# Performance work log

Measured on AMD Instinct MI355X. Metric: run time of the kernel, lower is better.

Reference implementation:

```python
import jax, jax.numpy as jnp
import numpy as np

UNITS = 128
N_CLASSES = 10
N_FEAT = 3
R_ON = 0.05      # time-gate open ratio
ALPHA = 0.001    # leak during closed phase
LN_EPS = 1e-3    # keras LayerNormalization default epsilon


def _time_gate(t, tau, s):
    # t: [B], tau/s: [U] -> k: [B, U]
    phi = jnp.mod(t[:, None] - s, tau) / tau
    k = jnp.where(phi < 0.5 * R_ON, 2.0 * phi / R_ON,
        jnp.where(phi < R_ON, 2.0 - 2.0 * phi / R_ON, ALPHA * phi))
    return k


def _plstm_step(x, t, h, c, Wx, Wh, b, tau, s):
    z = x @ Wx + h @ Wh + b                      # [B, 4U]
    i, f, g, o = jnp.split(z, 4, axis=-1)
    c_hat = jax.nn.sigmoid(f) * c + jax.nn.sigmoid(i) * jnp.tanh(g)
    h_hat = jax.nn.sigmoid(o) * jnp.tanh(c_hat)
    k = _time_gate(t, tau, s)
    return k * h_hat + (1.0 - k) * h, k * c_hat + (1.0 - k) * c


def _layer_norm(x, gamma, beta):
    mu = jnp.mean(x, axis=-1, keepdims=True)
    var = jnp.mean(jnp.square(x - mu), axis=-1, keepdims=True)
    return gamma * (x - mu) * jax.lax.rsqrt(var + LN_EPS) + beta


def setup_inputs() -> dict:
    key = jax.random.key(0)
    ks = jax.random.split(key, 16)
    B, T, F, U, C = 256, 1000, N_FEAT, UNITS, N_CLASSES
    inputs = jax.random.normal(ks[0], (B, T, F), dtype=jnp.float32)
    # strictly increasing-ish observation times per sequence
    times = jnp.cumsum(jax.random.uniform(ks[1], (B, T), dtype=jnp.float32), axis=1)
    sc_in = 1.0 / np.sqrt(F)
    sc_h = 1.0 / np.sqrt(U)
    Wx0 = jax.random.normal(ks[2], (F, 4 * U), dtype=jnp.float32) * sc_in
    Wh0 = jax.random.normal(ks[3], (U, 4 * U), dtype=jnp.float32) * sc_h
    b0 = jnp.zeros((4 * U,), dtype=jnp.float32)
    tau0 = jnp.exp(jax.random.uniform(ks[4], (U,), minval=0.0, maxval=3.0, dtype=jnp.float32))
    s0 = jax.random.uniform(ks[5], (U,), dtype=jnp.float32) * tau0
    Wx1 = jax.random.normal(ks[6], (U, 4 * U), dtype=jnp.float32) * sc_h
    Wh1 = jax.random.normal(ks[7], (U, 4 * U), dtype=jnp.float32) * sc_h
    b1 = jnp.zeros((4 * U,), dtype=jnp.float32)
    tau1 = jnp.exp(jax.random.uniform(ks[8], (U,), minval=0.0, maxval=3.0, dtype=jnp.float32))
    s1 = jax.random.uniform(ks[9], (U,), dtype=jnp.float32) * tau1
    gamma = jnp.ones((U,), dtype=jnp.float32)
    beta = jnp.zeros((U,), dtype=jnp.float32)
    Wfc = jax.random.normal(ks[10], (U, C), dtype=jnp.float32) * sc_h
    bfc = jnp.zeros((C,), dtype=jnp.float32)
    return {"inputs": inputs, "times": times, "Wx0": Wx0, "Wh0": Wh0, "b0": b0,
            "tau0": tau0, "s0": s0, "Wx1": Wx1, "Wh1": Wh1, "b1": b1,
            "tau1": tau1, "s1": s1, "gamma": gamma, "beta": beta,
            "Wfc": Wfc, "bfc": bfc}


def reference(inputs, times, Wx0, Wh0, b0, tau0, s0, Wx1, Wh1, b1, tau1, s1,
              gamma, beta, Wfc, bfc):
    B, T, F = inputs.shape
    U = Wh0.shape[0]
    x_t = jnp.transpose(inputs, (1, 0, 2))   # [T, B, F]
    t_t = jnp.transpose(times, (1, 0))       # [T, B]

    def step(carry, xt):
        h0, c0, h1, c1 = carry
        x, t = xt
        h0, c0 = _plstm_step(x, t, h0, c0, Wx0, Wh0, b0, tau0, s0)
        hn = _layer_norm(h0, gamma, beta)
        h1, c1 = _plstm_step(hn, t, h1, c1, Wx1, Wh1, b1, tau1, s1)
        probs = jax.nn.softmax(h1 @ Wfc + bfc, axis=-1)
        return (h0, c0, h1, c1), probs

    zeros = jnp.zeros((B, U), dtype=inputs.dtype)
    init = (zeros, zeros, zeros, zeros)
    _, out = jax.lax.scan(step, init, (x_t, t_t))  # out: [T, B, C]
    return jnp.transpose(out, (1, 0, 2))           # [B, T, C]
```

## Files before the change

kernel.cpp:

```cpp
#include <hip/hip_runtime.h>
#include <math.h>

constexpr int U      = 128;
constexpr int G4     = 512;
constexpr int NCls   = 10;
constexpr int TSTEPS = 1000;
constexpr int BATCH  = 256;
constexpr int CROWS  = 48;


__device__ __forceinline__ float sigm(float x) {
    return 1.0f / (1.0f + __expf(-x));
}

__device__ __forceinline__ float tgate(float t, float tau, float s) {
    float r = fmodf(t - s, tau);
    if (r < 0.0f) r += tau;
    const float phi = r / tau;
    return (phi < 0.025f) ? 40.0f * phi
         : (phi < 0.05f)  ? 2.0f - 40.0f * phi
         : 0.001f * phi;
}

#define ROW4(WP, I, HB) { \
    float4 w_; \
    w_ = (WP)[((I)+0)*128]; ac.x += (HB).x*w_.x; ac.y += (HB).x*w_.y; ac.z += (HB).x*w_.z; ac.w += (HB).x*w_.w; \
    w_ = (WP)[((I)+1)*128]; ac.x += (HB).y*w_.x; ac.y += (HB).y*w_.y; ac.z += (HB).y*w_.z; ac.w += (HB).y*w_.w; \
    w_ = (WP)[((I)+2)*128]; ac.x += (HB).z*w_.x; ac.y += (HB).z*w_.y; ac.z += (HB).z*w_.z; ac.w += (HB).z*w_.w; \
    w_ = (WP)[((I)+3)*128]; ac.x += (HB).w*w_.x; ac.y += (HB).w*w_.y; ac.z += (HB).w*w_.z; ac.w += (HB).w*w_.w; }

__global__ __launch_bounds__(1024, 1) void plstm_fused(
    const float* __restrict__ inputs,
    const float* __restrict__ times,
    const float* __restrict__ Wx0,
    const float* __restrict__ Wh0,
    const float* __restrict__ b0,
    const float* __restrict__ tau0,
    const float* __restrict__ s0,
    const float* __restrict__ Wx1,
    const float* __restrict__ Wh1,
    const float* __restrict__ b1,
    const float* __restrict__ tau1,
    const float* __restrict__ s1,
    const float* __restrict__ gamma_,
    const float* __restrict__ beta_,
    const float* __restrict__ Wfc,
    const float* __restrict__ bfc,
    float* __restrict__ out)
{
    const int tid = threadIdx.x;
    const int c4  = tid & 127;
    const int g   = tid >> 7;
    const int b   = blockIdx.x;

    __shared__ __align__(16) float wh0c[CROWS * G4];
    __shared__ __align__(16) float zu[8 * G4];
    __shared__ __align__(16) float h0s[U];
    __shared__ __align__(16) float ghu[2 * U];
    __shared__ __align__(16) float b0s[G4], b1s[G4], Ps[G4], Qs[G4];
    __shared__ __align__(16) float wx0s[3 * G4];
    __shared__ __align__(16) float wfcs[U * 11];
    __shared__ float bfcs[NCls];
    __shared__ float red[4];
    __shared__ float gms[U], bts[U];

    if (tid < U) { gms[tid] = gamma_[tid]; bts[tid] = beta_[tid];
                   h0s[tid] = 0.f; ghu[tid] = 0.f; ghu[U + tid] = 0.f; }
    {
        float4* dst = reinterpret_cast<float4*>(wh0c);
        const float4* src = reinterpret_cast<const float4*>(Wh0);
        #pragma unroll
        for (int i = 0; i < 6; ++i) dst[tid + i * 1024] = src[tid + i * 1024];
    }
    if (tid < G4) { b0s[tid] = b0[tid]; b1s[tid] = b1[tid]; }
    for (int i = tid; i < 3 * G4; i += 1024) wx0s[i] = Wx0[i];
    for (int i = tid; i < U * NCls; i += 1024) {
        const int u = i / NCls, c = i - u * NCls;
        wfcs[u * 11 + c] = Wfc[i];
    }
    if (tid < NCls) bfcs[tid] = bfc[tid];
    __syncthreads();

    if (tid < G4) {
        float P = 0.f, Q = 0.f;
        #pragma unroll 8
        for (int u = 0; u < U; ++u) {
            const float w = Wx1[u * G4 + tid];
            Q += gms[u] * w;
            P += bts[u] * w;
        }
        Ps[tid] = P; Qs[tid] = Q;
    }

    float tau0r = 0.f, s0r = 0.f, tau1r = 0.f, s1r = 0.f, gr = 0.f;
    if (tid < U) {
        tau0r = tau0[tid]; s0r = s0[tid];
        tau1r = tau1[tid]; s1r = s1[tid];
        gr = gms[tid];
    }
    float c0r = 0.f, c1r = 0.f, h0r = 0.f, h1r = 0.f;

    const float* __restrict__ xp = inputs + (size_t)b * TSTEPS * 3;
    const float* __restrict__ tp = times  + (size_t)b * TSTEPS;
    float*       __restrict__ op = out    + (size_t)b * TSTEPS * NCls;

    float xa0 = xp[0], xa1 = xp[1], xa2 = xp[2], tva = tp[0];

    __syncthreads();

    for (int t = 0; t < TSTEPS; ++t) {
        const float x0 = xa0, x1 = xa1, x2 = xa2, tv = tva;
        const int tn = (t + 1 < TSTEPS) ? t + 1 : t;
        xa0 = xp[tn*3+0]; xa1 = xp[tn*3+1]; xa2 = xp[tn*3+2]; tva = tp[tn];

        {
            float4 ac = make_float4(0.f, 0.f, 0.f, 0.f);
            const int r0 = g * 16;
            if (g < 3) {
                const float4* wp = reinterpret_cast<const float4*>(wh0c) + r0 * 128 + c4;
                #pragma unroll 2
                for (int i = 0; i < 16; i += 4) {
                    const float4 hb = *reinterpret_cast<const float4*>(&h0s[r0 + i]);
                    ROW4(wp, i, hb);
                }
            } else {
                const float4* wp = reinterpret_cast<const float4*>(Wh0) + r0 * 128 + c4;
                #pragma unroll 2
                for (int i = 0; i < 16; i += 4) {
                    const float4 hb = *reinterpret_cast<const float4*>(&h0s[r0 + i]);
                    ROW4(wp, i, hb);
                }
            }
            *reinterpret_cast<float4*>(&zu[g * G4 + 4 * c4]) = ac;
        }
        __syncthreads();

        if (tid < U) {
            const int u = tid;
            float z[4];
            #pragma unroll
            for (int q = 0; q < 4; ++q) {
                const int c = u + q * 128;
                float s = b0s[c] + x0 * wx0s[c] + x1 * wx0s[G4 + c] + x2 * wx0s[2 * G4 + c];
                #pragma unroll
                for (int gg = 0; gg < 8; ++gg) s += zu[gg * G4 + c];
                z[q] = s;
            }
            const float ig = sigm(z[0]);
            const float fg = sigm(z[1]);
            const float gg = tanhf(z[2]);
            const float og = sigm(z[3]);
            const float ch = fg * c0r + ig * gg;
            const float hh = og * tanhf(ch);
            const float k  = tgate(tv, tau0r, s0r);
            const float hn = k * hh + (1.0f - k) * h0r;
            c0r = k * ch + (1.0f - k) * c0r;
            h0r = hn;
            h0s[u] = hn;
            ghu[u] = gr * hn;
            float ssum = hn, qsum = hn * hn;
            #pragma unroll
            for (int off = 1; off < 64; off <<= 1) {
                ssum += __shfl_xor(ssum, off);
                qsum += __shfl_xor(qsum, off);
            }
            if ((tid & 63) == 0) {
                red[(tid >> 6) * 2]     = ssum;
                red[(tid >> 6) * 2 + 1] = qsum;
            }
        }
        __syncthreads();

        {
            const int half = tid >> 9;
            const int rg   = (tid >> 7) & 3;
            const int r0   = rg * 32;
            const float* __restrict__ Wm = half ? Wh1 : Wx1;
            const float* hvp = ghu + half * U + r0;
            const float4* wp = reinterpret_cast<const float4*>(Wm) + r0 * 128 + c4;
            float4 ac = make_float4(0.f, 0.f, 0.f, 0.f);
            #pragma unroll 2
            for (int i = 0; i < 32; i += 4) {
                const float4 hb = *reinterpret_cast<const float4*>(&hvp[i]);
                ROW4(wp, i, hb);
            }
            *reinterpret_cast<float4*>(&zu[(half * 4 + rg) * G4 + 4 * c4]) = ac;
        }
        __syncthreads();

        if (tid < U) {
            const float mu    = (red[0] + red[2]) * (1.0f / 128.0f);
            const float msq   = (red[1] + red[3]) * (1.0f / 128.0f);
            const float rstd  = rsqrtf(msq - mu * mu + 1e-3f);
            const float murstd = mu * rstd;
            const int u = tid;
            float z[4];
            #pragma unroll
            for (int q = 0; q < 4; ++q) {
                const int c = u + q * 128;
                const float sx = (zu[0*G4+c] + zu[1*G4+c]) + (zu[2*G4+c] + zu[3*G4+c]);
                const float sh = (zu[4*G4+c] + zu[5*G4+c]) + (zu[6*G4+c] + zu[7*G4+c]);
                z[q] = b1s[c] + Ps[c] + rstd * sx - murstd * Qs[c] + sh;
            }
            const float ig = sigm(z[0]);
            const float fg = sigm(z[1]);
            const float gg = tanhf(z[2]);
            const float og = sigm(z[3]);
            const float ch = fg * c1r + ig * gg;
            const float hh = og * tanhf(ch);
            const float k  = tgate(tv, tau1r, s1r);
            const float hn = k * hh + (1.0f - k) * h1r;
            c1r = k * ch + (1.0f - k) * c1r;
            h1r = hn;
            ghu[U + u] = hn;
        }
        __syncthreads();

        if (tid < 64) {
            const float a  = ghu[U + tid];
            const float bv = ghu[U + tid + 64];
            float p[NCls];
            #pragma unroll
            for (int c = 0; c < NCls; ++c)
                p[c] = a * wfcs[tid * 11 + c] + bv * wfcs[(tid + 64) * 11 + c];
            #pragma unroll
            for (int off = 1; off < 64; off <<= 1) {
                #pragma unroll
                for (int c = 0; c < NCls; ++c) p[c] += __shfl_xor(p[c], off);
            }
            float m = -1e30f;
            #pragma unroll
            for (int c = 0; c < NCls; ++c) { p[c] += bfcs[c]; m = fmaxf(m, p[c]); }
            float ssum = 0.0f;
            #pragma unroll
            for (int c = 0; c < NCls; ++c) { p[c] = __expf(p[c] - m); ssum += p[c]; }
            const float inv = 1.0f / ssum;
            float pv = p[0];
            #pragma unroll
            for (int c = 1; c < NCls; ++c) if (tid == c) pv = p[c];
            if (tid < NCls) op[t * NCls + tid] = pv * inv;
        }
    }
}

extern "C" void kernel_launch(void* const* d_in, const int* in_sizes, int n_in,
                              void* d_out, int out_size, void* d_ws, size_t ws_size,
                              hipStream_t stream) {
    const float* inputs = (const float*)d_in[0];
    const float* times  = (const float*)d_in[1];
    const float* Wx0    = (const float*)d_in[2];
    const float* Wh0    = (const float*)d_in[3];
    const float* b0     = (const float*)d_in[4];
    const float* tau0   = (const float*)d_in[5];
    const float* s0     = (const float*)d_in[6];
    const float* Wx1    = (const float*)d_in[7];
    const float* Wh1    = (const float*)d_in[8];
    const float* b1     = (const float*)d_in[9];
    const float* tau1   = (const float*)d_in[10];
    const float* s1     = (const float*)d_in[11];
    const float* gamma_ = (const float*)d_in[12];
    const float* beta_  = (const float*)d_in[13];
    const float* Wfc    = (const float*)d_in[14];
    const float* bfc    = (const float*)d_in[15];
    float* out = (float*)d_out;

    dim3 grid(BATCH);
    dim3 block(1024);
    hipLaunchKernelGGL(plstm_fused, grid, block, 0, stream,
                       inputs, times, Wx0, Wh0, b0, tau0, s0,
                       Wx1, Wh1, b1, tau1, s1, gamma_, beta_, Wfc, bfc, out);
}
```

Measured before the change: 7.087 ms.

## Prefetch global weight rows into registers before barriers and cache more Wh0 rows

Raises the number of Wh0 rows cached in shared memory from 48 to 56 and rebalances the row split: group 3 now takes rows 48-55 from shared memory plus rows 56-63 from preloaded registers. Groups that still read Wh0 from global memory issue the loads for their first 8 rows during the previous phase, before a barrier, so the latency overlaps other work. The same is done for the first 8 rows of Wx1/Wh1 in the layer-1 matvec, which are loaded before the barrier that precedes their use. This costs extra registers, about 64 floats per thread, and slightly more shared memory, which could cause spills at 1024 threads.

```diff
diff --git a/kernel.cpp b/kernel.cpp
--- a/kernel.cpp
+++ b/kernel.cpp
@@ -6,7 +6,7 @@
 constexpr int NCls   = 10;
 constexpr int TSTEPS = 1000;
 constexpr int BATCH  = 256;
-constexpr int CROWS  = 48;
+constexpr int CROWS  = 56;
 
 
 __device__ __forceinline__ float sigm(float x) {
@@ -28,6 +28,12 @@
     w_ = (WP)[((I)+1)*128]; ac.x += (HB).y*w_.x; ac.y += (HB).y*w_.y; ac.z += (HB).y*w_.z; ac.w += (HB).y*w_.w; \
     w_ = (WP)[((I)+2)*128]; ac.x += (HB).z*w_.x; ac.y += (HB).z*w_.y; ac.z += (HB).z*w_.z; ac.w += (HB).z*w_.w; \
     w_ = (WP)[((I)+3)*128]; ac.x += (HB).w*w_.x; ac.y += (HB).w*w_.y; ac.z += (HB).w*w_.z; ac.w += (HB).w*w_.w; }
+
+#define ROW4P(W0, W1, W2, W3, HB) { \
+    ac.x += (HB).x*(W0).x; ac.y += (HB).x*(W0).y; ac.z += (HB).x*(W0).z; ac.w += (HB).x*(W0).w; \
+    ac.x += (HB).y*(W1).x; ac.y += (HB).y*(W1).y; ac.z += (HB).y*(W1).z; ac.w += (HB).y*(W1).w; \
+    ac.x += (HB).z*(W2).x; ac.y += (HB).z*(W2).y; ac.z += (HB).z*(W2).z; ac.w += (HB).z*(W2).w; \
+    ac.x += (HB).w*(W3).x; ac.y += (HB).w*(W3).y; ac.z += (HB).w*(W3).z; ac.w += (HB).w*(W3).w; }
 
 __global__ __launch_bounds__(1024, 1) void plstm_fused(
     const float* __restrict__ inputs,
@@ -70,7 +76,7 @@
         float4* dst = reinterpret_cast<float4*>(wh0c);
         const float4* src = reinterpret_cast<const float4*>(Wh0);
         #pragma unroll
-        for (int i = 0; i < 6; ++i) dst[tid + i * 1024] = src[tid + i * 1024];
+        for (int i = 0; i < 7; ++i) dst[tid + i * 1024] = src[tid + i * 1024];
     }
     if (tid < G4) { b0s[tid] = b0[tid]; b1s[tid] = b1[tid]; }
     for (int i = tid; i < 3 * G4; i += 1024) wx0s[i] = Wx0[i];
@@ -100,11 +106,29 @@
     }
     float c0r = 0.f, c1r = 0.f, h0r = 0.f, h1r = 0.f;
 
+    const int paBase = (g == 3) ? 56 : g * 16;
+    const float4* __restrict__ wpA =
+        reinterpret_cast<const float4*>(Wh0) + paBase * 128 + c4;
+    const int half = tid >> 9;
+    const int rgC  = (tid >> 7) & 3;
+    const int r0C  = rgC * 32;
+    const float4* __restrict__ wpC =
+        reinterpret_cast<const float4*>(half ? Wh1 : Wx1) + r0C * 128 + c4;
+    const float* __restrict__ hvpC = ghu + half * U + r0C;
+
     const float* __restrict__ xp = inputs + (size_t)b * TSTEPS * 3;
     const float* __restrict__ tp = times  + (size_t)b * TSTEPS;
     float*       __restrict__ op = out    + (size_t)b * TSTEPS * NCls;
 
     float xa0 = xp[0], xa1 = xp[1], xa2 = xp[2], tva = tp[0];
+
+    float4 pa0, pa1, pa2, pa3, pa4, pa5, pa6, pa7;
+    if (g >= 3) {
+        pa0 = wpA[0 * 128]; pa1 = wpA[1 * 128];
+        pa2 = wpA[2 * 128]; pa3 = wpA[3 * 128];
+        pa4 = wpA[4 * 128]; pa5 = wpA[5 * 128];
+        pa6 = wpA[6 * 128]; pa7 = wpA[7 * 128];
+    }
 
     __syncthreads();
 
@@ -115,20 +139,33 @@
 
         {
             float4 ac = make_float4(0.f, 0.f, 0.f, 0.f);
-            const int r0 = g * 16;
             if (g < 3) {
-                const float4* wp = reinterpret_cast<const float4*>(wh0c) + r0 * 128 + c4;
-                #pragma unroll 2
+                const float4* wp = reinterpret_cast<const float4*>(wh0c) + g * 16 * 128 + c4;
+                #pragma unroll
                 for (int i = 0; i < 16; i += 4) {
-                    const float4 hb = *reinterpret_cast<const float4*>(&h0s[r0 + i]);
+                    const float4 hb = *reinterpret_cast<const float4*>(&h0s[g * 16 + i]);
                     ROW4(wp, i, hb);
                 }
             } else {
-                const float4* wp = reinterpret_cast<const float4*>(Wh0) + r0 * 128 + c4;
-                #pragma unroll 2
-                for (int i = 0; i < 16; i += 4) {
-                    const float4 hb = *reinterpret_cast<const float4*>(&h0s[r0 + i]);
-                    ROW4(wp, i, hb);
+                {
+                    const float4 hb0 = *reinterpret_cast<const float4*>(&h0s[paBase]);
+                    ROW4P(pa0, pa1, pa2, pa3, hb0);
+                    const float4 hb1 = *reinterpret_cast<const float4*>(&h0s[paBase + 4]);
+                    ROW4P(pa4, pa5, pa6, pa7, hb1);
+                }
+                if (g == 3) {
+                    const float4* wp = reinterpret_cast<const float4*>(wh0c) + 48 * 128 + c4;
+                    #pragma unroll
+                    for (int i = 0; i < 8; i += 4) {
+                        const float4 hb = *reinterpret_cast<const float4*>(&h0s[48 + i]);
+                        ROW4(wp, i, hb);
+                    }
+                } else {
+                    #pragma unroll
+                    for (int i = 8; i < 16; i += 4) {
+                        const float4 hb = *reinterpret_cast<const float4*>(&h0s[g * 16 + i]);
+                        ROW4(wpA, i, hb);
+                    }
                 }
             }
             *reinterpret_cast<float4*>(&zu[g * G4 + 4 * c4]) = ac;
@@ -169,22 +206,26 @@
                 red[(tid >> 6) * 2 + 1] = qsum;
             }
         }
+        const float4 pc0 = wpC[0 * 128], pc1 = wpC[1 * 128],
+                     pc2 = wpC[2 * 128], pc3 = wpC[3 * 128],
+                     pc4 = wpC[4 * 128], pc5 = wpC[5 * 128],
+                     pc6 = wpC[6 * 128], pc7 = wpC[7 * 128];
         __syncthreads();
 
         {
-            const int half = tid >> 9;
-            const int rg   = (tid >> 7) & 3;
-            const int r0   = rg * 32;
-            const float* __restrict__ Wm = half ? Wh1 : Wx1;
-            const float* hvp = ghu + half * U + r0;
-            const float4* wp = reinterpret_cast<const float4*>(Wm) + r0 * 128 + c4;
             float4 ac = make_float4(0.f, 0.f, 0.f, 0.f);
-            #pragma unroll 2
-            for (int i = 0; i < 32; i += 4) {
-                const float4 hb = *reinterpret_cast<const float4*>(&hvp[i]);
-                ROW4(wp, i, hb);
-            }
-            *reinterpret_cast<float4*>(&zu[(half * 4 + rg) * G4 + 4 * c4]) = ac;
+            {
+                const float4 hb0 = *reinterpret_cast<const float4*>(&hvpC[0]);
+                ROW4P(pc0, pc1, pc2, pc3, hb0);
+                const float4 hb1 = *reinterpret_cast<const float4*>(&hvpC[4]);
+                ROW4P(pc4, pc5, pc6, pc7, hb1);
+            }
+            #pragma unroll 3
+            for (int i = 8; i < 32; i += 4) {
+                const float4 hb = *reinterpret_cast<const float4*>(&hvpC[i]);
+                ROW4(wpC, i, hb);
+            }
+            *reinterpret_cast<float4*>(&zu[(half * 4 + rgC) * G4 + 4 * c4]) = ac;
         }
         __syncthreads();
 
@@ -213,6 +254,12 @@
             c1r = k * ch + (1.0f - k) * c1r;
             h1r = hn;
             ghu[U + u] = hn;
+        }
+        if (g >= 3) {
+            pa0 = wpA[0 * 128]; pa1 = wpA[1 * 128];
+            pa2 = wpA[2 * 128]; pa3 = wpA[3 * 128];
+            pa4 = wpA[4 * 128]; pa5 = wpA[5 * 128];
+            pa6 = wpA[6 * 128]; pa7 = wpA[7 * 128];
         }
         __syncthreads();
 
```

After: 15.54 ms. 2.19x slower.

## Software-pipeline layer-1 and softmax one step behind layer-0, cutting barriers per step

Applied to the files above, without the earlier changes.

Restructures the per-timestep schedule so layer-1's cell update and the softmax output for step t-1 run concurrently with layer-0's work for step t. All 16 wavefronts now do gate math: half handle layer 0 and half handle layer 1, each unit computed redundantly by paired wavefronts. Per-wave private h buffers (gh0w, h1w) and double zu buffers let the per-step barrier count drop from four to two. The shared-memory cache of Wh0 shrinks from 48 to 32 rows to make room for the extra buffers, so more Wh0 rows are read from global memory. The layer-norm statistics are now summed across duplicated wavefronts (hence the 1/256 divisor), and an epilogue finishes the last step.

```diff
diff --git a/kernel.cpp b/kernel.cpp
--- a/kernel.cpp
+++ b/kernel.cpp
@@ -6,7 +6,6 @@
 constexpr int NCls   = 10;
 constexpr int TSTEPS = 1000;
 constexpr int BATCH  = 256;
-constexpr int CROWS  = 48;
 
 
 __device__ __forceinline__ float sigm(float x) {
@@ -48,29 +47,37 @@
     const float* __restrict__ bfc,
     float* __restrict__ out)
 {
-    const int tid = threadIdx.x;
-    const int c4  = tid & 127;
-    const int g   = tid >> 7;
-    const int b   = blockIdx.x;
-
-    __shared__ __align__(16) float wh0c[CROWS * G4];
-    __shared__ __align__(16) float zu[8 * G4];
+    const int tid  = threadIdx.x;
+    const int lane = tid & 63;
+    const int wv   = tid >> 6;
+    const int c4   = tid & 127;
+    const int g    = tid >> 7;
+    const int half = tid >> 9;
+    const int rgC  = (tid >> 7) & 3;
+    const int b    = blockIdx.x;
+
+    __shared__ __align__(16) float wh0c[32 * G4];
+    __shared__ __align__(16) float zu0[8 * G4];
+    __shared__ __align__(16) float zu1[8 * G4];
     __shared__ __align__(16) float h0s[U];
-    __shared__ __align__(16) float ghu[2 * U];
+    __shared__ __align__(16) float h1s[U];
+    __shared__ __align__(16) float gh0w[8][32];
+    __shared__ __align__(16) float h1w[8][32];
     __shared__ __align__(16) float b0s[G4], b1s[G4], Ps[G4], Qs[G4];
     __shared__ __align__(16) float wx0s[3 * G4];
     __shared__ __align__(16) float wfcs[U * 11];
     __shared__ float bfcs[NCls];
-    __shared__ float red[4];
+    __shared__ float red[8];
     __shared__ float gms[U], bts[U];
 
     if (tid < U) { gms[tid] = gamma_[tid]; bts[tid] = beta_[tid];
-                   h0s[tid] = 0.f; ghu[tid] = 0.f; ghu[U + tid] = 0.f; }
+                   h0s[tid] = 0.f; h1s[tid] = 0.f; }
+    if (tid < 256) { ((float*)h1w)[tid] = 0.f; }
     {
         float4* dst = reinterpret_cast<float4*>(wh0c);
         const float4* src = reinterpret_cast<const float4*>(Wh0);
         #pragma unroll
-        for (int i = 0; i < 6; ++i) dst[tid + i * 1024] = src[tid + i * 1024];
+        for (int i = 0; i < 4; ++i) dst[tid + i * 1024] = src[tid + i * 1024];
     }
     if (tid < G4) { b0s[tid] = b0[tid]; b1s[tid] = b1[tid]; }
     for (int i = tid; i < 3 * G4; i += 1024) wx0s[i] = Wx0[i];
@@ -92,19 +99,28 @@
         Ps[tid] = P; Qs[tid] = Q;
     }
 
-    float tau0r = 0.f, s0r = 0.f, tau1r = 0.f, s1r = 0.f, gr = 0.f;
-    if (tid < U) {
-        tau0r = tau0[tid]; s0r = s0[tid];
-        tau1r = tau1[tid]; s1r = s1[tid];
-        gr = gms[tid];
-    }
-    float c0r = 0.f, c1r = 0.f, h0r = 0.f, h1r = 0.f;
+    const int rg0 = (half == 0) ? (wv >> 1) : 0;
+    const int rg1 = (half == 1) ? ((wv - 8) >> 1) : 0;
+    const int um  = ((half == 0) ? rg0 : rg1) * 32 + (lane & 31);
+    float tauM = 0.f, sM = 0.f, grM = 0.f;
+    if (half == 0) { tauM = tau0[um]; sM = s0[um]; grM = gamma_[um]; }
+    else           { tauM = tau1[um]; sM = s1[um]; }
+    float cM = 0.f, hM = 0.f;
+
+    const float4* __restrict__ wpA =
+        reinterpret_cast<const float4*>(Wh0) + g * 16 * 128 + c4;
+    const float4* __restrict__ wpAc =
+        reinterpret_cast<const float4*>(wh0c) + g * 16 * 128 + c4;
+    const float4* __restrict__ wpC =
+        reinterpret_cast<const float4*>(half ? Wh1 : Wx1) + rgC * 32 * 128 + c4;
+    const float* __restrict__ hvC = half ? &h1w[wv - 8][0] : &gh0w[wv][0];
 
     const float* __restrict__ xp = inputs + (size_t)b * TSTEPS * 3;
     const float* __restrict__ tp = times  + (size_t)b * TSTEPS;
     float*       __restrict__ op = out    + (size_t)b * TSTEPS * NCls;
 
     float xa0 = xp[0], xa1 = xp[1], xa2 = xp[2], tva = tp[0];
+    float tvp = 0.f;
 
     __syncthreads();
 
@@ -113,133 +129,150 @@
         const int tn = (t + 1 < TSTEPS) ? t + 1 : t;
         xa0 = xp[tn*3+0]; xa1 = xp[tn*3+1]; xa2 = xp[tn*3+2]; tva = tp[tn];
 
+        if (half == 1 && t > 0) {
+            const float mu   = (red[0]+red[2]+red[4]+red[6]) * (1.0f/256.0f);
+            const float msq  = (red[1]+red[3]+red[5]+red[7]) * (1.0f/256.0f);
+            const float rstd = rsqrtf(msq - mu*mu + 1e-3f);
+            const float murstd = mu * rstd;
+            float z[4];
+            #pragma unroll
+            for (int q = 0; q < 4; ++q) {
+                const int c = um + q * 128;
+                const float sx = (zu1[0*G4+c] + zu1[1*G4+c]) + (zu1[2*G4+c] + zu1[3*G4+c]);
+                const float sh = (zu1[4*G4+c] + zu1[5*G4+c]) + (zu1[6*G4+c] + zu1[7*G4+c]);
+                z[q] = b1s[c] + Ps[c] + rstd * sx - murstd * Qs[c] + sh;
+            }
+            const float ig = sigm(z[0]), fg = sigm(z[1]);
+            const float gg = tanhf(z[2]), og = sigm(z[3]);
+            const float ch = fg * cM + ig * gg;
+            const float hh = og * tanhf(ch);
+            const float k  = tgate(tvp, tauM, sM);
+            const float hn = k * hh + (1.0f - k) * hM;
+            cM = k * ch + (1.0f - k) * cM;
+            hM = hn;
+            if (lane < 32) { h1w[wv - 8][lane] = hn; h1s[um] = hn; }
+        }
         {
             float4 ac = make_float4(0.f, 0.f, 0.f, 0.f);
-            const int r0 = g * 16;
-            if (g < 3) {
-                const float4* wp = reinterpret_cast<const float4*>(wh0c) + r0 * 128 + c4;
-                #pragma unroll 2
-                for (int i = 0; i < 16; i += 4) {
-                    const float4 hb = *reinterpret_cast<const float4*>(&h0s[r0 + i]);
-                    ROW4(wp, i, hb);
-                }
-            } else {
-                const float4* wp = reinterpret_cast<const float4*>(Wh0) + r0 * 128 + c4;
-                #pragma unroll 2
-                for (int i = 0; i < 16; i += 4) {
-                    const float4 hb = *reinterpret_cast<const float4*>(&h0s[r0 + i]);
-                    ROW4(wp, i, hb);
-                }
-            }
-            *reinterpret_cast<float4*>(&zu[g * G4 + 4 * c4]) = ac;
+            const float4* wp = (g < 2) ? wpAc : wpA;
+            #pragma unroll
+            for (int i = 0; i < 16; i += 4) {
+                const float4 hb = *reinterpret_cast<const float4*>(&h0s[g * 16 + i]);
+                ROW4(wp, i, hb);
+            }
+            *reinterpret_cast<float4*>(&zu0[g * G4 + 4 * c4]) = ac;
         }
         __syncthreads();
 
-        if (tid < U) {
-            const int u = tid;
+        if (wv == 0 && t > 0) {
+            const float a  = h1s[lane];
+            const float bv = h1s[lane + 64];
+            float p[NCls];
+            #pragma unroll
+            for (int c = 0; c < NCls; ++c)
+                p[c] = a * wfcs[lane * 11 + c] + bv * wfcs[(lane + 64) * 11 + c];
+            #pragma unroll
+            for (int off = 1; off < 64; off <<= 1) {
+                #pragma unroll
+                for (int c = 0; c < NCls; ++c) p[c] += __shfl_xor(p[c], off);
+            }
+            float m = -1e30f;
+            #pragma unroll
+            for (int c = 0; c < NCls; ++c) { p[c] += bfcs[c]; m = fmaxf(m, p[c]); }
+            float ssum = 0.0f;
+            #pragma unroll
+            for (int c = 0; c < NCls; ++c) { p[c] = __expf(p[c] - m); ssum += p[c]; }
+            const float inv = 1.0f / ssum;
+            float pv = p[0];
+            #pragma unroll
+            for (int c = 1; c < NCls; ++c) if (lane == c) pv = p[c];
+            if (lane < NCls) op[(t - 1) * NCls + lane] = pv * inv;
+        }
+        if (half == 0) {
             float z[4];
             #pragma unroll
             for (int q = 0; q < 4; ++q) {
-                const int c = u + q * 128;
-                float s = b0s[c] + x0 * wx0s[c] + x1 * wx0s[G4 + c] + x2 * wx0s[2 * G4 + c];
-                #pragma unroll
-                for (int gg = 0; gg < 8; ++gg) s += zu[gg * G4 + c];
+                const int c = um + q * 128;
+                float s = b0s[c] + x0 * wx0s[c] + x1 * wx0s[G4 + c] + x2 * wx0s[2*G4 + c];
+                s += (zu0[0*G4+c] + zu0[1*G4+c]) + (zu0[2*G4+c] + zu0[3*G4+c]);
+                s += (zu0[4*G4+c] + zu0[5*G4+c]) + (zu0[6*G4+c] + zu0[7*G4+c]);
                 z[q] = s;
             }
-            const float ig = sigm(z[0]);
-            const float fg = sigm(z[1]);
-            const float gg = tanhf(z[2]);
-            const float og = sigm(z[3]);
-            const float ch = fg * c0r + ig * gg;
+            const float ig = sigm(z[0]), fg = sigm(z[1]);
+            const float gg = tanhf(z[2]), og = sigm(z[3]);
+            const float ch = fg * cM + ig * gg;
             const float hh = og * tanhf(ch);
-            const float k  = tgate(tv, tau0r, s0r);
-            const float hn = k * hh + (1.0f - k) * h0r;
-            c0r = k * ch + (1.0f - k) * c0r;
-            h0r = hn;
-            h0s[u] = hn;
-            ghu[u] = gr * hn;
+            const float k  = tgate(tv, tauM, sM);
+            const float hn = k * hh + (1.0f - k) * hM;
+            cM = k * ch + (1.0f - k) * cM;
+            hM = hn;
+            if (lane < 32) { h0s[um] = hn; gh0w[wv][lane] = grM * hn; }
             float ssum = hn, qsum = hn * hn;
             #pragma unroll
             for (int off = 1; off < 64; off <<= 1) {
                 ssum += __shfl_xor(ssum, off);
                 qsum += __shfl_xor(qsum, off);
             }
-            if ((tid & 63) == 0) {
-                red[(tid >> 6) * 2]     = ssum;
-                red[(tid >> 6) * 2 + 1] = qsum;
-            }
-        }
+            if (lane == 0) { red[2 * rg0] = ssum; red[2 * rg0 + 1] = qsum; }
+        }
+        {
+            float4 ac = make_float4(0.f, 0.f, 0.f, 0.f);
+            #pragma unroll 4
+            for (int i = 0; i < 32; i += 4) {
+                const float4 hb = *reinterpret_cast<const float4*>(&hvC[i]);
+                ROW4(wpC, i, hb);
+            }
+            *reinterpret_cast<float4*>(&zu1[(half * 4 + rgC) * G4 + 4 * c4]) = ac;
+        }
+        tvp = tv;
         __syncthreads();
-
-        {
-            const int half = tid >> 9;
-            const int rg   = (tid >> 7) & 3;
-            const int r0   = rg * 32;
-            const float* __restrict__ Wm = half ? Wh1 : Wx1;
-            const float* hvp = ghu + half * U + r0;
-            const float4* wp = reinterpret_cast<const float4*>(Wm) + r0 * 128 + c4;
-            float4 ac = make_float4(0.f, 0.f, 0.f, 0.f);
-            #pragma unroll 2
-            for (int i = 0; i < 32; i += 4) {
-                const float4 hb = *reinterpret_cast<const float4*>(&hvp[i]);
-                ROW4(wp, i, hb);
-            }
-            *reinterpret_cast<float4*>(&zu[(half * 4 + rg) * G4 + 4 * c4]) = ac;
-        }
-        __syncthreads();
-
-        if (tid < U) {
-            const float mu    = (red[0] + red[2]) * (1.0f / 128.0f);
-            const float msq   = (red[1] + red[3]) * (1.0f / 128.0f);
-            const float rstd  = rsqrtf(msq - mu * mu + 1e-3f);
-            const float murstd = mu * rstd;
-            const int u = tid;
-            float z[4];
-            #pragma unroll
-            for (int q = 0; q < 4; ++q) {
-                const int c = u + q * 128;
-                const float sx = (zu[0*G4+c] + zu[1*G4+c]) + (zu[2*G4+c] + zu[3*G4+c]);
-                const float sh = (zu[4*G4+c] + zu[5*G4+c]) + (zu[6*G4+c] + zu[7*G4+c]);
-                z[q] = b1s[c] + Ps[c] + rstd * sx - murstd * Qs[c] + sh;
-            }
-            const float ig = sigm(z[0]);
-            const float fg = sigm(z[1]);
-            const float gg = tanhf(z[2]);
-            const float og = sigm(z[3]);
-            const float ch = fg * c1r + ig * gg;
-            const float hh = og * tanhf(ch);
-            const float k  = tgate(tv, tau1r, s1r);
-            const float hn = k * hh + (1.0f - k) * h1r;
-            c1r = k * ch + (1.0f - k) * c1r;
-            h1r = hn;
-            ghu[U + u] = hn;
-        }
-        __syncthreads();
-
-        if (tid < 64) {
-            const float a  = ghu[U + tid];
-            const float bv = ghu[U + tid + 64];
-            float p[NCls];
-            #pragma unroll
-            for (int c = 0; c < NCls; ++c)
-                p[c] = a * wfcs[tid * 11 + c] + bv * wfcs[(tid + 64) * 11 + c];
-            #pragma unroll
-            for (int off = 1; off < 64; off <<= 1) {
-                #pragma unroll
-                for (int c = 0; c < NCls; ++c) p[c] += __shfl_xor(p[c], off);
-            }
-            float m = -1e30f;
-            #pragma unroll
-            for (int c = 0; c < NCls; ++c) { p[c] += bfcs[c]; m = fmaxf(m, p[c]); }
-            float ssum = 0.0f;
-            #pragma unroll
-            for (int c = 0; c < NCls; ++c) { p[c] = __expf(p[c] - m); ssum += p[c]; }
-            const float inv = 1.0f / ssum;
-            float pv = p[0];
-            #pragma unroll
-            for (int c = 1; c < NCls; ++c) if (tid == c) pv = p[c];
-            if (tid < NCls) op[t * NCls + tid] = pv * inv;
-        }
+    }
+
+    if (half == 1) {
+        const float mu   = (red[0]+red[2]+red[4]+red[6]) * (1.0f/256.0f);
+        const float msq  = (red[1]+red[3]+red[5]+red[7]) * (1.0f/256.0f);
+        const float rstd = rsqrtf(msq - mu*mu + 1e-3f);
+        const float murstd = mu * rstd;
+        float z[4];
+        #pragma unroll
+        for (int q = 0; q < 4; ++q) {
+            const int c = um + q * 128;
+            const float sx = (zu1[0*G4+c] + zu1[1*G4+c]) + (zu1[2*G4+c] + zu1[3*G4+c]);
+            const float sh = (zu1[4*G4+c] + zu1[5*G4+c]) + (zu1[6*G4+c] + zu1[7*G4+c]);
+            z[q] = b1s[c] + Ps[c] + rstd * sx - murstd * Qs[c] + sh;
+        }
+        const float ig = sigm(z[0]), fg = sigm(z[1]);
+        const float gg = tanhf(z[2]), og = sigm(z[3]);
+        const float ch = fg * cM + ig * gg;
+        const float hh = og * tanhf(ch);
+        const float k  = tgate(tvp, tauM, sM);
+        const float hn = k * hh + (1.0f - k) * hM;
+        if (lane < 32) h1s[um] = hn;
+    }
+    __syncthreads();
+    if (wv == 0) {
+        const float a  = h1s[lane];
+        const float bv = h1s[lane + 64];
+        float p[NCls];
+        #pragma unroll
+        for (int c = 0; c < NCls; ++c)
+            p[c] = a * wfcs[lane * 11 + c] + bv * wfcs[(lane + 64) * 11 + c];
+        #pragma unroll
+        for (int off = 1; off < 64; off <<= 1) {
+            #pragma unroll
+            for (int c = 0; c < NCls; ++c) p[c] += __shfl_xor(p[c], off);
+        }
+        float m = -1e30f;
+        #pragma unroll
+        for (int c = 0; c < NCls; ++c) { p[c] += bfcs[c]; m = fmaxf(m, p[c]); }
+        float ssum = 0.0f;
+        #pragma unroll
+        for (int c = 0; c < NCls; ++c) { p[c] = __expf(p[c] - m); ssum += p[c]; }
+        const float inv = 1.0f / ssum;
+        float pv = p[0];
+        #pragma unroll
+        for (int c = 1; c < NCls; ++c) if (lane == c) pv = p[c];
+        if (lane < NCls) op[(TSTEPS - 1) * NCls + lane] = pv * inv;
     }
 }
 
```

New measurement: 9.452 ms. 1.33x slower.

## Overlap layer-1 recurrent matvec with layer-0 update and merge final phases

Applied to the files above, without the earlier changes.

Threads in the upper half compute the Wh1·h1 partial products during the same barrier interval as the layer-0 gate update, since h1 is already known from the previous step; the lower half computes the Wx1 part afterwards. Layer-1 gate computation and the softmax output are merged into a single wavefront handling two units per lane, which removes one block-wide barrier per step. The first weight row of each slice is hoisted into registers and separate accumulation buffers are used. The cost is more register pressure and uneven per-phase work between the two halves.

```diff
diff --git a/kernel.cpp b/kernel.cpp
--- a/kernel.cpp
+++ b/kernel.cpp
@@ -48,13 +48,18 @@
     const float* __restrict__ bfc,
     float* __restrict__ out)
 {
-    const int tid = threadIdx.x;
-    const int c4  = tid & 127;
-    const int g   = tid >> 7;
-    const int b   = blockIdx.x;
+    const int tid  = threadIdx.x;
+    const int lane = tid & 63;
+    const int wv   = tid >> 6;
+    const int c4   = tid & 127;
+    const int g    = tid >> 7;
+    const int half = tid >> 9;
+    const int rgC  = (tid >> 7) & 3;
+    const int b    = blockIdx.x;
 
     __shared__ __align__(16) float wh0c[CROWS * G4];
-    __shared__ __align__(16) float zu[8 * G4];
+    __shared__ __align__(16) float zuA[8 * G4];
+    __shared__ __align__(16) float zuB[8 * G4];
     __shared__ __align__(16) float h0s[U];
     __shared__ __align__(16) float ghu[2 * U];
     __shared__ __align__(16) float b0s[G4], b1s[G4], Ps[G4], Qs[G4];
@@ -92,13 +97,22 @@
         Ps[tid] = P; Qs[tid] = Q;
     }
 
-    float tau0r = 0.f, s0r = 0.f, tau1r = 0.f, s1r = 0.f, gr = 0.f;
-    if (tid < U) {
-        tau0r = tau0[tid]; s0r = s0[tid];
-        tau1r = tau1[tid]; s1r = s1[tid];
-        gr = gms[tid];
-    }
-    float c0r = 0.f, c1r = 0.f, h0r = 0.f, h1r = 0.f;
+    float tau0r = 0.f, s0r = 0.f, gr = 0.f;
+    if (tid < U) { tau0r = tau0[tid]; s0r = s0[tid]; gr = gms[tid]; }
+    float tau1A = 0.f, s1A = 0.f, tau1B = 0.f, s1B = 0.f;
+    if (wv == 0) { tau1A = tau1[lane]; s1A = s1[lane];
+                   tau1B = tau1[lane + 64]; s1B = s1[lane + 64]; }
+    float c0r = 0.f, h0r = 0.f;
+    float c1A = 0.f, h1A = 0.f, c1B = 0.f, h1B = 0.f;
+
+    const float4* __restrict__ wpA  =
+        reinterpret_cast<const float4*>(Wh0) + g * 16 * 128 + c4;
+    const float4* __restrict__ wpAc =
+        reinterpret_cast<const float4*>(wh0c) + g * 16 * 128 + c4;
+    const float4* __restrict__ wpC  =
+        reinterpret_cast<const float4*>(half ? Wh1 : Wx1) + rgC * 32 * 128 + c4;
+    const float* __restrict__ hvC = ghu + half * U + rgC * 32;
+    const float4 pc = wpC[0];
 
     const float* __restrict__ xp = inputs + (size_t)b * TSTEPS * 3;
     const float* __restrict__ tp = times  + (size_t)b * TSTEPS;
@@ -115,23 +129,13 @@
 
         {
             float4 ac = make_float4(0.f, 0.f, 0.f, 0.f);
-            const int r0 = g * 16;
-            if (g < 3) {
-                const float4* wp = reinterpret_cast<const float4*>(wh0c) + r0 * 128 + c4;
-                #pragma unroll 2
-                for (int i = 0; i < 16; i += 4) {
-                    const float4 hb = *reinterpret_cast<const float4*>(&h0s[r0 + i]);
-                    ROW4(wp, i, hb);
-                }
-            } else {
-                const float4* wp = reinterpret_cast<const float4*>(Wh0) + r0 * 128 + c4;
-                #pragma unroll 2
-                for (int i = 0; i < 16; i += 4) {
-                    const float4 hb = *reinterpret_cast<const float4*>(&h0s[r0 + i]);
-                    ROW4(wp, i, hb);
-                }
-            }
-            *reinterpret_cast<float4*>(&zu[g * G4 + 4 * c4]) = ac;
+            const float4* wp = (g < 3) ? wpAc : wpA;
+            #pragma unroll
+            for (int i = 0; i < 16; i += 4) {
+                const float4 hb = *reinterpret_cast<const float4*>(&h0s[g * 16 + i]);
+                ROW4(wp, i, hb);
+            }
+            *reinterpret_cast<float4*>(&zuA[g * G4 + 4 * c4]) = ac;
         }
         __syncthreads();
 
@@ -143,13 +147,11 @@
                 const int c = u + q * 128;
                 float s = b0s[c] + x0 * wx0s[c] + x1 * wx0s[G4 + c] + x2 * wx0s[2 * G4 + c];
                 #pragma unroll
-                for (int gg = 0; gg < 8; ++gg) s += zu[gg * G4 + c];
+                for (int gg = 0; gg < 8; ++gg) s += zuA[gg * G4 + c];
                 z[q] = s;
             }
-            const float ig = sigm(z[0]);
-            const float fg = sigm(z[1]);
-            const float gg = tanhf(z[2]);
-            const float og = sigm(z[3]);
+            const float ig = sigm(z[0]), fg = sigm(z[1]);
+            const float gg = tanhf(z[2]), og = sigm(z[3]);
             const float ch = fg * c0r + ig * gg;
             const float hh = og * tanhf(ch);
             const float k  = tgate(tv, tau0r, s0r);
@@ -169,60 +171,80 @@
                 red[(tid >> 6) * 2 + 1] = qsum;
             }
         }
+        if (half == 1) {
+            float4 ac = make_float4(0.f, 0.f, 0.f, 0.f);
+            {
+                const float4 hb = *reinterpret_cast<const float4*>(&hvC[0]);
+                ac.x += hb.x * pc.x; ac.y += hb.x * pc.y;
+                ac.z += hb.x * pc.z; ac.w += hb.x * pc.w;
+                float4 w_;
+                w_ = wpC[1 * 128]; ac.x += hb.y*w_.x; ac.y += hb.y*w_.y; ac.z += hb.y*w_.z; ac.w += hb.y*w_.w;
+                w_ = wpC[2 * 128]; ac.x += hb.z*w_.x; ac.y += hb.z*w_.y; ac.z += hb.z*w_.z; ac.w += hb.z*w_.w;
+                w_ = wpC[3 * 128]; ac.x += hb.w*w_.x; ac.y += hb.w*w_.y; ac.z += hb.w*w_.z; ac.w += hb.w*w_.w;
+            }
+            #pragma unroll
+            for (int i = 4; i < 32; i += 4) {
+                const float4 hb = *reinterpret_cast<const float4*>(&hvC[i]);
+                ROW4(wpC, i, hb);
+            }
+            *reinterpret_cast<float4*>(&zuB[(4 + rgC) * G4 + 4 * c4]) = ac;
+        }
         __syncthreads();
 
-        {
-            const int half = tid >> 9;
-            const int rg   = (tid >> 7) & 3;
-            const int r0   = rg * 32;
-            const float* __restrict__ Wm = half ? Wh1 : Wx1;
-            const float* hvp = ghu + half * U + r0;
-            const float4* wp = reinterpret_cast<const float4*>(Wm) + r0 * 128 + c4;
+        if (half == 0) {
             float4 ac = make_float4(0.f, 0.f, 0.f, 0.f);
-            #pragma unroll 2
-            for (int i = 0; i < 32; i += 4) {
-                const float4 hb = *reinterpret_cast<const float4*>(&hvp[i]);
-                ROW4(wp, i, hb);
-            }
-            *reinterpret_cast<float4*>(&zu[(half * 4 + rg) * G4 + 4 * c4]) = ac;
+            {
+                const float4 hb = *reinterpret_cast<const float4*>(&hvC[0]);
+                ac.x += hb.x * pc.x; ac.y += hb.x * pc.y;
+                ac.z += hb.x * pc.z; ac.w += hb.x * pc.w;
+                float4 w_;
+                w_ = wpC[1 * 128]; ac.x += hb.y*w_.x; ac.y += hb.y*w_.y; ac.z += hb.y*w_.z; ac.w += hb.y*w_.w;
+                w_ = wpC[2 * 128]; ac.x += hb.z*w_.x; ac.y += hb.z*w_.y; ac.z += hb.z*w_.z; ac.w += hb.z*w_.w;
+                w_ = wpC[3 * 128]; ac.x += hb.w*w_.x; ac.y += hb.w*w_.y; ac.z += hb.w*w_.z; ac.w += hb.w*w_.w;
+            }
+            #pragma unroll
+            for (int i = 4; i < 32; i += 4) {
+                const float4 hb = *reinterpret_cast<const float4*>(&hvC[i]);
+                ROW4(wpC, i, hb);
+            }
+            *reinterpret_cast<float4*>(&zuB[rgC * G4 + 4 * c4]) = ac;
         }
         __syncthreads();
 
-        if (tid < U) {
+        if (wv == 0) {
             const float mu    = (red[0] + red[2]) * (1.0f / 128.0f);
             const float msq   = (red[1] + red[3]) * (1.0f / 128.0f);
             const float rstd  = rsqrtf(msq - mu * mu + 1e-3f);
             const float murstd = mu * rstd;
-            const int u = tid;
-            float z[4];
-            #pragma unroll
-            for (int q = 0; q < 4; ++q) {
-                const int c = u + q * 128;
-                const float sx = (zu[0*G4+c] + zu[1*G4+c]) + (zu[2*G4+c] + zu[3*G4+c]);
-                const float sh = (zu[4*G4+c] + zu[5*G4+c]) + (zu[6*G4+c] + zu[7*G4+c]);
-                z[q] = b1s[c] + Ps[c] + rstd * sx - murstd * Qs[c] + sh;
-            }
-            const float ig = sigm(z[0]);
-            const float fg = sigm(z[1]);
-            const float gg = tanhf(z[2]);
-            const float og = sigm(z[3]);
-            const float ch = fg * c1r + ig * gg;
-            const float hh = og * tanhf(ch);
-            const float k  = tgate(tv, tau1r, s1r);
-            const float hn = k * hh + (1.0f - k) * h1r;
-            c1r = k * ch + (1.0f - k) * c1r;
-            h1r = hn;
-            ghu[U + u] = hn;
-        }
-        __syncthreads();
-
-        if (tid < 64) {
-            const float a  = ghu[U + tid];
-            const float bv = ghu[U + tid + 64];
+            float hnv[2];
+            #pragma unroll
+            for (int e = 0; e < 2; ++e) {
+                const int u = lane + e * 64;
+                float z[4];
+                #pragma unroll
+                for (int q = 0; q < 4; ++q) {
+                    const int c = u + q * 128;
+                    const float sx = (zuB[0*G4+c] + zuB[1*G4+c]) + (zuB[2*G4+c] + zuB[3*G4+c]);
+                    const float sh = (zuB[4*G4+c] + zuB[5*G4+c]) + (zuB[6*G4+c] + zuB[7*G4+c]);
+                    z[q] = b1s[c] + Ps[c] + rstd * sx - murstd * Qs[c] + sh;
+                }
+                const float ig = sigm(z[0]), fg = sigm(z[1]);
+                const float gg = tanhf(z[2]), og = sigm(z[3]);
+                const float cprev = e ? c1B : c1A;
+                const float hprev = e ? h1B : h1A;
+                const float ch = fg * cprev + ig * gg;
+                const float hh = og * tanhf(ch);
+                const float k  = tgate(tv, e ? tau1B : tau1A, e ? s1B : s1A);
+                const float hn = k * hh + (1.0f - k) * hprev;
+                if (e) { c1B = k * ch + (1.0f - k) * c1B; h1B = hn; }
+                else   { c1A = k * ch + (1.0f - k) * c1A; h1A = hn; }
+                ghu[U + u] = hn;
+                hnv[e] = hn;
+            }
             float p[NCls];
             #pragma unroll
             for (int c = 0; c < NCls; ++c)
-                p[c] = a * wfcs[tid * 11 + c] + bv * wfcs[(tid + 64) * 11 + c];
+                p[c] = hnv[0] * wfcs[lane * 11 + c] + hnv[1] * wfcs[(lane + 64) * 11 + c];
             #pragma unroll
             for (int off = 1; off < 64; off <<= 1) {
                 #pragma unroll
@@ -237,8 +259,8 @@
             const float inv = 1.0f / ssum;
             float pv = p[0];
             #pragma unroll
-            for (int c = 1; c < NCls; ++c) if (tid == c) pv = p[c];
-            if (tid < NCls) op[t * NCls + tid] = pv * inv;
+            for (int c = 1; c < NCls; ++c) if (lane == c) pv = p[c];
+            if (lane < NCls) op[t * NCls + lane] = pv * inv;
         }
     }
 }
```

New measurement: 27.85 ms. 3.93x slower.
